# Kernel tuning notes

Measured on AMD Instinct MI355X. Metric: run time of the kernel, lower is better.

The kernel has to match this reference:

```python
import jax, jax.numpy as jnp
import numpy as np

B, N, D_PATCH = 32, 196, 768
TKN, QK, H, HID = 768, 64, 12, 3072
K_STEPS = 12
ALPHA = 1.0
BETA = 1.0 / (QK ** 0.5)
EPS = 1e-5


def setup_inputs() -> dict:
    key = jax.random.key(0)
    ks = jax.random.split(key, 8)
    w_std = 0.002
    return {
        "x": jax.random.normal(ks[0], (B, N, D_PATCH), jnp.float32),
        "w_enc": jax.random.normal(ks[1], (TKN, D_PATCH), jnp.float32) * 0.02,
        "b_enc": jnp.zeros((TKN,), jnp.float32),
        "cls_tok": jnp.ones((1, 1, TKN), jnp.float32),
        "pos": jax.random.normal(ks[2], (1, N + 1, TKN), jnp.float32) * w_std,
        "eln_gamma": jnp.ones((1,), jnp.float32),
        "eln_bias": jnp.zeros((TKN,), jnp.float32),
        "wq": jax.random.normal(ks[3], (H, QK, TKN), jnp.float32) * w_std,
        "wk": jax.random.normal(ks[4], (H, QK, TKN), jnp.float32) * w_std,
        "w_hop": jax.random.normal(ks[5], (HID, TKN), jnp.float32) * 0.02,
        "dec_ln_w": jnp.ones((TKN,), jnp.float32),
        "dec_ln_b": jnp.zeros((TKN,), jnp.float32),
        "w_dec": jax.random.normal(ks[6], (D_PATCH, TKN), jnp.float32) * 0.02,
        "b_dec": jnp.zeros((D_PATCH,), jnp.float32),
    }


def _energy(g, wq, wk, w_hop):
    # attention energy: non-softmax, -1/beta * sum logsumexp(beta * A)
    q = jnp.einsum('bnd,hzd->bnhz', g, wq)
    k = jnp.einsum('bnd,hzd->bnhz', g, wk)
    A = jnp.einsum('bqhz,bkhz->bhqk', q, k)  # [B,H,N+1,N+1]
    e_attn = (-1.0 / BETA) * jnp.sum(jax.nn.logsumexp(BETA * A, axis=-1))
    # Hopfield energy: -0.5 * sum relu(g W^T)^2
    h = jnp.einsum('bnd,fd->bnf', g, w_hop)  # [B,N+1,HID]
    e_hop = -0.5 * jnp.sum(jax.nn.relu(h) ** 2)
    return e_attn + e_hop


def _energy_ln(x, gamma, bias):
    xm = x - x.mean(-1, keepdims=True)
    o = xm / jnp.sqrt((xm ** 2).mean(-1, keepdims=True) + EPS)
    return gamma * o + bias


def _layernorm(x, w, b):
    mu = x.mean(-1, keepdims=True)
    xm = x - mu
    var = (xm ** 2).mean(-1, keepdims=True)
    return xm / jnp.sqrt(var + EPS) * w + b


def reference(x, w_enc, b_enc, cls_tok, pos, eln_gamma, eln_bias,
              wq, wk, w_hop, dec_ln_w, dec_ln_b, w_dec, b_dec):
    # encode: Linear(d_patch -> tkn)
    t = jnp.einsum('bnd,td->bnt', x, w_enc) + b_enc
    # prepend cls, add positional encoding
    cls = jnp.broadcast_to(cls_tok, (t.shape[0], 1, TKN))
    t = jnp.concatenate([cls, t], axis=1) + pos  # [B, N+1, TKN]

    grad_e = jax.grad(lambda g: _energy(g, wq, wk, w_hop))
    for _ in range(K_STEPS):  # fixed unroll over time steps (single block)
        g = _energy_ln(t, eln_gamma, eln_bias)
        t = t - ALPHA * grad_e(g)

    # decode: LayerNorm + Linear(tkn -> d_patch)
    y = _layernorm(t, dec_ln_w, dec_ln_b)
    y = jnp.einsum('bnt,dt->bnd', y, w_dec) + b_dec
    return y[:, 1:]  # drop cls token (use_cls=False)
```

## Files before the change

### kernel.cpp

```cpp
#include <hip/hip_runtime.h>
#include <hip/hip_bf16.h>

typedef __hip_bfloat16 bf16;
typedef short s8 __attribute__((ext_vector_type(8)));
typedef short sv4 __attribute__((ext_vector_type(4)));
typedef float f4 __attribute__((ext_vector_type(4)));

#define BETA 0.125f
#define EPS 1e-5f

__device__ __forceinline__ void gld16(const void* g, void* l){
    __builtin_amdgcn_global_load_lds(
        (const __attribute__((address_space(1))) void*)g,
        (__attribute__((address_space(3))) void*)l, 16, 0, 0);
}

__global__ __launch_bounds__(256) void f2b_k(const float* __restrict__ in, bf16* __restrict__ out, long n){
    long i = (long)blockIdx.x*256 + threadIdx.x;
    if (i < n) out[i] = __float2bfloat16(in[i]);
}
__global__ __launch_bounds__(256) void padx_k(const float* __restrict__ x, bf16* __restrict__ xb){
    long i = (long)blockIdx.x*256 + threadIdx.x;
    if (i >= 6400L*768) return;
    long row = i / 768;
    xb[i] = (row < 6272) ? __float2bfloat16(x[i]) : __float2bfloat16(0.f);
}
__global__ __launch_bounds__(256) void tr_k(const short* __restrict__ Bi, short* __restrict__ Bo){
    __shared__ short t[32][33];
    int i0 = blockIdx.x*32, j0 = blockIdx.y*32;
    int li = threadIdx.x & 31, lj = threadIdx.x >> 5;
    #pragma unroll
    for (int r=0;r<4;r++) t[lj+8*r][li] = Bi[(long)(i0+lj+8*r)*768 + j0+li];
    __syncthreads();
    #pragma unroll
    for (int r=0;r<4;r++) Bo[(long)(j0+lj+8*r)*4608 + i0+li] = t[li][lj+8*r];
}

__global__ __launch_bounds__(256) void cls_k(const float* __restrict__ cls, const float* __restrict__ pos,
                                             float* __restrict__ t){
    int i = blockIdx.x*256 + threadIdx.x;
    int b = i / 768, c = i % 768;
    t[((long)b*197)*768 + c] = cls[c] + pos[c];
}

template<int MODE>
__global__ __launch_bounds__(256) void big_gemm(
    const short* __restrict__ A, int lda,
    const short* __restrict__ B, int ldb,
    float* __restrict__ Cf, bf16* __restrict__ Cb, int ldc,
    int K, int Nn, int Nm, int relu0, long zoff,
    const float* __restrict__ bias, const float* __restrict__ pos)
{
    const int f = blockIdx.x;
    const int npg = 16*Nn;
    const int grp = f / npg;
    const int first_m = grp*16;
    const int gs = (Nm - first_m < 16) ? (Nm - first_m) : 16;
    const int rem = f % npg;
    const int bm = first_m + rem % gs;
    const int bn = rem / gs;

    __shared__ short lsA[8192];
    __shared__ short lsB[8192];
    const int tid = threadIdx.x;
    const int w = tid>>6, l = tid&63;
    const int m0 = bm*128, n0 = bn*128;
    const int srow = tid>>2;
    const int qglob = ((tid&3) - (tid>>3)) & 3;
    const int scol = qglob*8;
    int koff, Ks;
    if (MODE==1){ Ks = K>>1; koff = blockIdx.z * Ks; Cf += (size_t)blockIdx.z * zoff; }
    else        { Ks = K;    koff = 0; }
    const short* pa = A + (size_t)(m0+srow)*lda + koff + scol;
    const short* pb = B + (size_t)(n0+srow)*ldb + koff + scol;
    short* laP = lsA + w*512;
    short* lbP = lsB + w*512;
    const int wm = (w>>1)*64, wn = (w&1)*64;
    const int fr = l&15, fq = ((l>>4) + (fr>>1) & 3)*8;
    f4 acc[4][4] = {};
    const int nk = Ks>>6;
    for (int kt=0; kt<nk; kt++){
        const size_t ko = (size_t)kt*64;
        const size_t ra = 64*(size_t)lda, rb = 64*(size_t)ldb;
        gld16(pa + ko,           laP);
        gld16(pa + ko + ra,      laP + 2048);
        gld16(pa + ko + 32,      laP + 4096);
        gld16(pa + ko + 32 + ra, laP + 6144);
        gld16(pb + ko,           lbP);
        gld16(pb + ko + rb,      lbP + 2048);
        gld16(pb + ko + 32,      lbP + 4096);
        gld16(pb + ko + 32 + rb, lbP + 6144);
        __syncthreads();
        #pragma unroll
        for (int ks=0; ks<2; ks++){
            s8 af[4], bfr[4];
            #pragma unroll
            for (int i=0;i<4;i++) af[i]  = *(const s8*)(lsA + ks*4096 + (wm+i*16+fr)*32 + fq);
            #pragma unroll
            for (int j=0;j<4;j++) bfr[j] = *(const s8*)(lsB + ks*4096 + (wn+j*16+fr)*32 + fq);
            #pragma unroll
            for (int i=0;i<4;i++)
                #pragma unroll
                for (int j=0;j<4;j++)
                    acc[i][j] = __builtin_amdgcn_mfma_f32_16x16x32_bf16(af[i], bfr[j], acc[i][j], 0,0,0);
        }
        __syncthreads();
    }
    const int er = (l>>4)*4;
    const int ec = l&15;
    #pragma unroll
    for (int i=0;i<4;i++){
        #pragma unroll
        for (int j=0;j<4;j++){
            int gr0 = m0 + wm + i*16 + er;
            int gc  = n0 + wn + j*16 + ec;
            #pragma unroll
            for (int r=0;r<4;r++){
                float v = acc[i][j][r];
                int gr = gr0 + r;
                if (MODE==0){
                    if (gc >= relu0) v = v>0.f ? v : 0.f;
                    Cb[(size_t)gr*ldc + gc] = __float2bfloat16(v);
                } else if (MODE==1){
                    Cf[(size_t)gr*ldc + gc] = v;
                } else if (MODE==2){
                    if (gr < 6272){
                        int b = gr/196, n = gr%196;
                        Cf[((size_t)b*197 + n + 1)*768 + gc] = v + bias[gc] + pos[(long)(n+1)*768+gc];
                    }
                } else {
                    if (gr < 6272) Cf[(size_t)gr*ldc + gc] = v + bias[gc];
                }
            }
        }
    }
}

template<int MODE>
__global__ __launch_bounds__(256, 2) void wide_gemm(
    const short* __restrict__ A, int lda,
    const short* __restrict__ B, int ldb,
    float* __restrict__ Cf, float* __restrict__ Cf2,
    bf16* __restrict__ Cb, int ldc,
    int K, int Nn, int Nm, int relu0, long zoff)
{
    const int f = blockIdx.x;
    const int npg = 16*Nn;
    const int grp = f / npg;
    const int first_m = grp*16;
    const int gs = (Nm - first_m < 16) ? (Nm - first_m) : 16;
    const int rem = f % npg;
    const int bm = first_m + rem % gs;
    const int bn = rem / gs;

    __shared__ short lsA[16384];
    __shared__ short lsB[8192];
    const int tid = threadIdx.x;
    const int w = tid>>6, l = tid&63;
    const int m0 = bm*256, n0 = bn*128;

    int Ks, koff; float* Cp = Cf;
    if (MODE==1){ Ks = K/3; koff = blockIdx.z * Ks;
                  Cp = (blockIdx.z==2) ? Cf2 : Cf + (size_t)blockIdx.z * zoff; }
    else        { Ks = K; koff = 0; }
    const int NT = Ks>>5;

    const short* sA[4]; const short* sB[2];
    #pragma unroll
    for (int j=0;j<4;j++){
        int c = j*256 + tid;
        int r = c>>2, qd = c&3;
        int qs = (qd - (r>>1)) & 3;
        sA[j] = A + (size_t)(m0+r)*lda + koff + qs*8;
    }
    #pragma unroll
    for (int j=0;j<2;j++){
        int c = j*256 + tid;
        int r = c>>2, qd = c&3;
        int qs = (qd - (r>>1)) & 3;
        sB[j] = B + (size_t)(n0+r)*ldb + koff + qs*8;
    }

    const int wm = (w>>1)*128, wn = (w&1)*64;
    const int fr = l&15;
    const int fq = (((l>>4) + (fr>>1)) & 3)*8;
    f4 acc[8][4] = {};

    short* dA0 = lsA + w*512;
    short* dB0 = lsB + w*512;

    #pragma unroll
    for (int j=0;j<4;j++) gld16(sA[j], dA0 + j*2048);
    #pragma unroll
    for (int j=0;j<2;j++) gld16(sB[j], dB0 + j*2048);
    __syncthreads();

    int buf = 0;
    for (int t=0; t<NT; t++){
        if (t+1 < NT){
            const size_t ko = (size_t)(t+1)*32;
            short* dA = dA0 + (buf^1)*8192;
            short* dB = dB0 + (buf^1)*4096;
            #pragma unroll
            for (int j=0;j<4;j++) gld16(sA[j]+ko, dA + j*2048);
            #pragma unroll
            for (int j=0;j<2;j++) gld16(sB[j]+ko, dB + j*2048);
        }
        __builtin_amdgcn_sched_barrier(0);
        const short* aP = lsA + buf*8192;
        const short* bP = lsB + buf*4096;
        s8 af[8], bfr[4];
        #pragma unroll
        for (int i=0;i<8;i++) af[i]  = *(const s8*)(aP + (wm+i*16+fr)*32 + fq);
        #pragma unroll
        for (int j=0;j<4;j++) bfr[j] = *(const s8*)(bP + (wn+j*16+fr)*32 + fq);
        __builtin_amdgcn_s_setprio(1);
        #pragma unroll
        for (int i=0;i<8;i++)
            #pragma unroll
            for (int j=0;j<4;j++)
                acc[i][j] = __builtin_amdgcn_mfma_f32_16x16x32_bf16(af[i], bfr[j], acc[i][j], 0,0,0);
        __builtin_amdgcn_s_setprio(0);
        __syncthreads();
        buf ^= 1;
    }

    const int er = (l>>4)*4;
    const int ec = l&15;
    #pragma unroll
    for (int i=0;i<8;i++){
        #pragma unroll
        for (int j=0;j<4;j++){
            int gr0 = m0 + wm + i*16 + er;
            int gc  = n0 + wn + j*16 + ec;
            #pragma unroll
            for (int r=0;r<4;r++){
                float v = acc[i][j][r];
                int gr = gr0 + r;
                if (MODE==0){
                    if (gc >= relu0) v = v>0.f ? v : 0.f;
                    Cb[(size_t)gr*ldc + gc] = __float2bfloat16(v);
                } else {
                    Cp[(size_t)gr*ldc + gc] = v;
                }
            }
        }
    }
}

__global__ __launch_bounds__(256) void pack_k(const short* __restrict__ qkh,
                                              short* __restrict__ qT, short* __restrict__ kT){
    __shared__ short tq[64][65];
    __shared__ short tk[64][65];
    const int bh = blockIdx.x, b = bh/12, h = bh%12;
    const int mc = blockIdx.y*64;
    const int tid = threadIdx.x;
    #pragma unroll
    for (int e=0;e<16;e++){
        int i = tid + e*256; int r = i>>6, c = i&63;
        int mg = mc + r;
        short vq = 0, vk = 0;
        if (mg < 197){
            size_t base = (size_t)(b*197+mg)*4608 + h*64 + c;
            vq = qkh[base]; vk = qkh[base+768];
        }
        tq[r][c] = vq; tk[r][c] = vk;
    }
    __syncthreads();
    #pragma unroll
    for (int e=0;e<16;e++){
        int i = tid + e*256; int zr = i>>6, cm = i&63;
        size_t o = (size_t)bh*16384 + (size_t)zr*256 + mc + cm;
        qT[o] = tq[cm][zr];
        kT[o] = tk[cm][zr];
    }
}

__global__ __launch_bounds__(256) void attn_k(
    short* __restrict__ qkh, const short* __restrict__ qT, const short* __restrict__ kT)
{
    __shared__ short Pl[64*232];
    __shared__ short Ptl[208*72];
    const int bh = blockIdx.x, b = bh/12, h = bh%12;
    const int tid = threadIdx.x, w = tid>>6, l = tid&63;
    const int lr = l&15, lq = l>>4;
    const size_t qcol = (size_t)h*64, kcol = 768 + qcol;
    const size_t rbase = (size_t)b*197*4608;
    const short* qTp = qT + (size_t)bh*16384;
    const short* kTp = kT + (size_t)bh*16384;

    for (int i=tid; i<64*16; i+=256){ int r=i>>4, c=208+(i&15); Pl[r*232+c]=0; }

    f4 ak[13];
    #pragma unroll
    for (int t=0;t<13;t++) ak[t] = (f4){0.f,0.f,0.f,0.f};

    for (int iter=0; iter<4; iter++){
        const int m0 = iter*64;
        f4 S[13];
        #pragma unroll
        for (int t=0;t<13;t++) S[t] = (f4){0.f,0.f,0.f,0.f};
        const int mrow = m0 + w*16 + lr;
        #pragma unroll
        for (int ks=0; ks<2; ks++){
            s8 af = *(const s8*)(qkh + rbase + (size_t)mrow*4608 + qcol + ks*32 + lq*8);
            #pragma unroll
            for (int t=0;t<13;t++){
                s8 bf = *(const s8*)(qkh + rbase + (size_t)(t*16+lr)*4608 + kcol + ks*32 + lq*8);
                S[t] = __builtin_amdgcn_mfma_f32_16x16x32_bf16(af, bf, S[t], 0,0,0);
            }
        }
        __syncthreads();
        const int mbase = w*16 + lq*4;
        #pragma unroll
        for (int r=0;r<4;r++){
            float mx = -1e30f;
            #pragma unroll
            for (int t=0;t<13;t++){
                float v = S[t][r]*BETA;
                if (t==12 && lr>=5) v = -1e30f;
                S[t][r] = v;
                mx = fmaxf(mx, v);
            }
            mx = fmaxf(mx, __shfl_xor(mx,1,64)); mx = fmaxf(mx, __shfl_xor(mx,2,64));
            mx = fmaxf(mx, __shfl_xor(mx,4,64)); mx = fmaxf(mx, __shfl_xor(mx,8,64));
            float sm = 0.f;
            #pragma unroll
            for (int t=0;t<13;t++){ float e = __expf(S[t][r]-mx); S[t][r]=e; sm+=e; }
            sm += __shfl_xor(sm,1,64); sm += __shfl_xor(sm,2,64);
            sm += __shfl_xor(sm,4,64); sm += __shfl_xor(sm,8,64);
            float inv = 1.f/sm;
            bool valid = (m0 + mbase + r) < 197;
            #pragma unroll
            for (int t=0;t<13;t++) S[t][r] = valid ? S[t][r]*inv : 0.f;
        }
        #pragma unroll
        for (int t=0;t<13;t++){
            int c = t*16 + lr;
            short pb[4];
            #pragma unroll
            for (int r=0;r<4;r++){
                bf16 bv = __float2bfloat16(S[t][r]);
                pb[r] = *(short*)&bv;
                Pl[(mbase+r)*232 + c] = pb[r];
            }
            *(sv4*)(Ptl + c*72 + mbase) = (sv4){pb[0],pb[1],pb[2],pb[3]};
        }
        __syncthreads();
        f4 aq[4];
        #pragma unroll
        for (int t=0;t<4;t++) aq[t] = (f4){0.f,0.f,0.f,0.f};
        #pragma unroll
        for (int ks=0; ks<7; ks++){
            s8 af = *(const s8*)(kTp + (w*16+lr)*256 + ks*32 + lq*8);
            #pragma unroll
            for (int mt=0;mt<4;mt++){
                s8 bf = *(const s8*)(Pl + (mt*16+lr)*232 + ks*32 + lq*8);
                aq[mt] = __builtin_amdgcn_mfma_f32_16x16x32_bf16(af, bf, aq[mt], 0,0,0);
            }
        }
        #pragma unroll
        for (int mt=0;mt<4;mt++){
            int mg = m0 + mt*16 + lr;
            if (mg < 197){
                sv4 pv;
                #pragma unroll
                for (int r=0;r<4;r++){ bf16 bv=__float2bfloat16(aq[mt][r]); pv[r]=*(short*)&bv; }
                *(sv4*)(qkh + rbase + (size_t)mg*4608 + qcol + w*16 + lq*4) = pv;
            }
        }
        #pragma unroll
        for (int ks=0; ks<2; ks++){
            s8 bf = *(const s8*)(qTp + (w*16+lr)*256 + m0 + ks*32 + lq*8);
            #pragma unroll
            for (int t=0;t<13;t++){
                s8 af = *(const s8*)(Ptl + (t*16+lr)*72 + ks*32 + lq*8);
                ak[t] = __builtin_amdgcn_mfma_f32_16x16x32_bf16(af, bf, ak[t], 0,0,0);
            }
        }
    }
    #pragma unroll
    for (int t=0;t<13;t++){
        #pragma unroll
        for (int r=0;r<4;r++){
            int n = t*16 + lq*4 + r;
            if (n < 197)
                *(bf16*)(qkh + rbase + (size_t)n*4608 + kcol + w*16 + lr) = __float2bfloat16(ak[t][r]);
        }
    }
}

__global__ __launch_bounds__(256) void ln_k(
    float* __restrict__ in, bf16* __restrict__ out,
    const float* __restrict__ p0, const float* __restrict__ p1, const float* __restrict__ p2,
    const float* __restrict__ scale, const float* __restrict__ bias,
    int scalar_scale, int rowmap, int addp, int writet)
{
    int r = blockIdx.x;
    long src = rowmap ? ((long)(r/196)*197 + r%196 + 1) : (long)r;
    float* xr = in + src*768;
    int tid = threadIdx.x;
    float v0 = xr[tid], v1 = xr[tid+256], v2 = xr[tid+512];
    if (addp){
        const float* a = p0 + src*768;
        const float* b = p1 + src*768;
        const float* c = p2 + src*768;
        v0 += a[tid]     + b[tid]     + c[tid];
        v1 += a[tid+256] + b[tid+256] + c[tid+256];
        v2 += a[tid+512] + b[tid+512] + c[tid+512];
        if (writet){ xr[tid]=v0; xr[tid+256]=v1; xr[tid+512]=v2; }
    }
    __shared__ float red[4];
    float s = v0+v1+v2;
    #pragma unroll
    for (int o=1;o<64;o<<=1) s += __shfl_xor(s, o, 64);
    if ((tid&63)==0) red[tid>>6] = s;
    __syncthreads();
    float mu = (red[0]+red[1]+red[2]+red[3]) * (1.f/768.f);
    float d0=v0-mu, d1=v1-mu, d2=v2-mu;
    float q = d0*d0 + d1*d1 + d2*d2;
    #pragma unroll
    for (int o=1;o<64;o<<=1) q += __shfl_xor(q, o, 64);
    __syncthreads();
    if ((tid&63)==0) red[tid>>6] = q;
    __syncthreads();
    float ms = (red[0]+red[1]+red[2]+red[3]) * (1.f/768.f);
    float inv = rsqrtf(ms + EPS);
    bf16* o_ = out + (long)r*768;
    float s0 = scalar_scale ? scale[0] : scale[tid];
    float s1 = scalar_scale ? s0 : scale[tid+256];
    float s2 = scalar_scale ? s0 : scale[tid+512];
    o_[tid]     = __float2bfloat16(d0*inv*s0 + bias[tid]);
    o_[tid+256] = __float2bfloat16(d1*inv*s1 + bias[tid+256]);
    o_[tid+512] = __float2bfloat16(d2*inv*s2 + bias[tid+512]);
}

extern "C" void kernel_launch(void* const* d_in, const int* in_sizes, int n_in,
                              void* d_out, int out_size, void* d_ws, size_t ws_size,
                              hipStream_t stream) {
    const float* x       = (const float*)d_in[0];
    const float* w_enc   = (const float*)d_in[1];
    const float* b_enc   = (const float*)d_in[2];
    const float* cls_tok = (const float*)d_in[3];
    const float* pos     = (const float*)d_in[4];
    const float* eln_g   = (const float*)d_in[5];
    const float* eln_b   = (const float*)d_in[6];
    const float* wq      = (const float*)d_in[7];
    const float* wk      = (const float*)d_in[8];
    const float* w_hop   = (const float*)d_in[9];
    const float* dln_w   = (const float*)d_in[10];
    const float* dln_b   = (const float*)d_in[11];
    const float* w_dec   = (const float*)d_in[12];
    const float* b_dec   = (const float*)d_in[13];
    float* out = (float*)d_out;

    float* t_  = (float*)d_ws;
    bf16* g_   = (bf16*)(t_ + 6400L*768);
    bf16* qkh  = g_ + 6400L*768;
    bf16* qT   = qkh + 6400L*4608;
    bf16* kT   = qT + 384L*16384;
    float* p0  = (float*)(kT + 384L*16384);
    float* p1  = p0 + 6400L*768;
    bf16* B1   = (bf16*)(p1 + 6400L*768);
    bf16* B2   = B1 + 4608L*768;
    bf16* we_  = B2 + 768L*4608;
    bf16* wd_  = we_ + 768L*768;
    float* p2  = (float*)qT;

    dim3 blk(256);
    const long ZOFF = 6400L*768;

    f2b_k<<<dim3((589824+255)/256),  blk, 0, stream>>>(wq,    B1,          589824);
    f2b_k<<<dim3((589824+255)/256),  blk, 0, stream>>>(wk,    B1+589824,   589824);
    f2b_k<<<dim3((2359296+255)/256), blk, 0, stream>>>(w_hop, B1+1179648, 2359296);
    f2b_k<<<dim3((589824+255)/256),  blk, 0, stream>>>(w_enc, we_,         589824);
    f2b_k<<<dim3((589824+255)/256),  blk, 0, stream>>>(w_dec, wd_,         589824);
    tr_k<<<dim3(144,24), blk, 0, stream>>>((const short*)B1, (short*)B2);
    padx_k<<<dim3((int)((6400L*768+255)/256)), blk, 0, stream>>>(x, g_);

    cls_k<<<dim3(96), blk, 0, stream>>>(cls_tok, pos, t_);
    big_gemm<2><<<dim3(300), blk, 0, stream>>>((const short*)g_, 768, (const short*)we_, 768,
                                               t_, nullptr, 768, 768, 6, 50, 0, 0, b_enc, pos);

    for (int step=0; step<12; step++){
        ln_k<<<dim3(6304), blk, 0, stream>>>(t_, g_, p0, p1, p2, eln_g, eln_b, 1, 0, step>0, 1);
        wide_gemm<0><<<dim3(900), blk, 0, stream>>>((const short*)g_, 768, (const short*)B1, 768,
                                                    nullptr, nullptr, qkh, 4608, 768, 36, 25, 1536, 0);
        pack_k<<<dim3(384,4), blk, 0, stream>>>((const short*)qkh, (short*)qT, (short*)kT);
        attn_k<<<dim3(384), blk, 0, stream>>>((short*)qkh, (const short*)qT, (const short*)kT);
        wide_gemm<1><<<dim3(150,1,3), blk, 0, stream>>>((const short*)qkh, 4608, (const short*)B2, 4608,
                                                        p0, p2, nullptr, 768, 4608, 6, 25, 0, ZOFF);
    }

    ln_k<<<dim3(6272), blk, 0, stream>>>(t_, g_, p0, p1, p2, dln_w, dln_b, 0, 1, 1, 0);
    big_gemm<3><<<dim3(300), blk, 0, stream>>>((const short*)g_, 768, (const short*)wd_, 768,
                                               out, nullptr, 768, 768, 6, 50, 0, 0, b_dec, nullptr);
}
```

Baseline: 2.586 ms.

## Triple-buffer LDS in wide GEMM with explicit vmcnt waits

Changes the wide GEMM main loop from double to triple buffering of the A/B tiles in LDS, issuing loads two K-steps ahead. Syncthreads is replaced with partial s_waitcnt vmcnt(6) plus raw s_barrier, so loads for the next-next stage stay in flight during MFMA work. It also drops the setprio hints. LDS use rises from 48KB to 72KB per block, which can cut occupancy under launch_bounds(256,2). It also relies on hand-counted vmcnt values and on the barrier ordering to avoid overwriting a buffer that is still being read.

```diff
diff --git a/kernel.cpp b/kernel.cpp
--- a/kernel.cpp
+++ b/kernel.cpp
@@ -153,8 +153,8 @@
     const int bm = first_m + rem % gs;
     const int bn = rem / gs;
 
-    __shared__ short lsA[16384];
-    __shared__ short lsB[8192];
+    __shared__ short lsA[24576];
+    __shared__ short lsB[12288];
     const int tid = threadIdx.x;
     const int w = tid>>6, l = tid&63;
     const int m0 = bm*256, n0 = bn*128;
@@ -186,44 +186,45 @@
     const int fq = (((l>>4) + (fr>>1)) & 3)*8;
     f4 acc[8][4] = {};
 
-    short* dA0 = lsA + w*512;
-    short* dB0 = lsB + w*512;
-
-    #pragma unroll
-    for (int j=0;j<4;j++) gld16(sA[j], dA0 + j*2048);
-    #pragma unroll
-    for (int j=0;j<2;j++) gld16(sB[j], dB0 + j*2048);
-    __syncthreads();
-
-    int buf = 0;
+    #define STAGE(T, SL) do{ \
+        const size_t ko_ = (size_t)(T)*32; \
+        short* dA_ = lsA + (SL)*8192 + w*512; \
+        short* dB_ = lsB + (SL)*4096 + w*512; \
+        gld16(sA[0]+ko_, dA_);       gld16(sA[1]+ko_, dA_+2048); \
+        gld16(sA[2]+ko_, dA_+4096);  gld16(sA[3]+ko_, dA_+6144); \
+        gld16(sB[0]+ko_, dB_);       gld16(sB[1]+ko_, dB_+2048); \
+    }while(0)
+
+    STAGE(0, 0);
+    if (NT > 1){ STAGE(1, 1); asm volatile("s_waitcnt vmcnt(6)" ::: "memory"); }
+    else       { asm volatile("s_waitcnt vmcnt(0)" ::: "memory"); }
+    __builtin_amdgcn_s_barrier();
+
+    int s = 0;
     for (int t=0; t<NT; t++){
-        if (t+1 < NT){
-            const size_t ko = (size_t)(t+1)*32;
-            short* dA = dA0 + (buf^1)*8192;
-            short* dB = dB0 + (buf^1)*4096;
-            #pragma unroll
-            for (int j=0;j<4;j++) gld16(sA[j]+ko, dA + j*2048);
-            #pragma unroll
-            for (int j=0;j<2;j++) gld16(sB[j]+ko, dB + j*2048);
-        }
-        __builtin_amdgcn_sched_barrier(0);
-        const short* aP = lsA + buf*8192;
-        const short* bP = lsB + buf*4096;
+        if (t+2 < NT){
+            int s2 = s+2; if (s2>=3) s2 -= 3;
+            STAGE(t+2, s2);
+        }
+        const short* aP = lsA + s*8192;
+        const short* bP = lsB + s*4096;
         s8 af[8], bfr[4];
         #pragma unroll
         for (int i=0;i<8;i++) af[i]  = *(const s8*)(aP + (wm+i*16+fr)*32 + fq);
         #pragma unroll
         for (int j=0;j<4;j++) bfr[j] = *(const s8*)(bP + (wn+j*16+fr)*32 + fq);
-        __builtin_amdgcn_s_setprio(1);
         #pragma unroll
         for (int i=0;i<8;i++)
             #pragma unroll
             for (int j=0;j<4;j++)
                 acc[i][j] = __builtin_amdgcn_mfma_f32_16x16x32_bf16(af[i], bfr[j], acc[i][j], 0,0,0);
-        __builtin_amdgcn_s_setprio(0);
-        __syncthreads();
-        buf ^= 1;
-    }
+        if (t == NT-1) break;
+        if (t+2 < NT) asm volatile("s_waitcnt vmcnt(6)" ::: "memory");
+        else          asm volatile("s_waitcnt vmcnt(0)" ::: "memory");
+        __builtin_amdgcn_s_barrier();
+        s = (s==2) ? 0 : s+1;
+    }
+    #undef STAGE
 
     const int er = (l>>4)*4;
     const int ec = l&15;
```

Result: slower. 2.649 ms (+2.5%).
